# Performance work log

Measured on AMD Instinct MI355X. Metric: run time of the kernel, lower is better.

The kernel has to match this reference:

```python
import jax, jax.numpy as jnp
import numpy as np

# LIF hyperparameters (match init_kwargs)
DT = 1.0
TAU = 20.0
THRESHOLD = 1.0
RESET = 0.0
REST = 0.0
REFR_PERIOD = 2.0
LOW_BOUND = -1.0
KOEFF = float(np.exp(-DT / TAU))  # membrane decay per step
N = 2048
N_IN = 512
N_OUT = 256
B = 64
T = 512


def setup_inputs() -> dict:
    key = jax.random.key(0)
    k1, k2 = jax.random.split(key)
    # Binary input spike trains [B, n_in, T] (uint8 semantics, stored as float32)
    inp = (jax.random.uniform(k1, (B, N_IN, T)) < 0.2).astype(jnp.float32)
    # Dense synaptic weight matrix W [N, N]; row i = incoming weights of neuron i
    W = jax.random.normal(k2, (N, N), dtype=jnp.float32) * (0.1 / np.sqrt(N))
    return {"inp": inp, "W": W}


def reference(inp, W):
    batch, n_in, time = inp.shape
    n = W.shape[0]
    xs = jnp.moveaxis(inp, 2, 0)  # [T, B, n_in]

    def step(carry, x_t):
        state, refr, out_t = carry  # state/refr/out_t: [B, N]
        # Inject input spikes into the first n_in output slots
        out_t = out_t.at[:, :n_in].set(x_t)
        # LIF update: decay toward rest + synaptic input W @ out_t
        state = (state - REST) * KOEFF + REST + jnp.einsum('ij,bj->bi', W, out_t)
        # Refractory neurons clamped to reset potential
        state = jnp.where(refr > 0, RESET, state)
        spike = state >= THRESHOLD
        refr = refr - DT
        refr = jnp.where(spike, REFR_PERIOD, refr)
        # Lower-bound clamp on membrane potential
        state = jnp.where(state < LOW_BOUND, LOW_BOUND, state)
        out_t = spike.astype(jnp.float32)
        return (state, refr, out_t), out_t[:, -N_OUT:]

    init = (jnp.zeros((batch, n), jnp.float32),
            jnp.zeros((batch, n), jnp.float32),
            jnp.zeros((batch, n), jnp.float32))
    _, outs = jax.lax.scan(step, init, xs)  # outs: [T, B, n_out]
    return jnp.transpose(outs, (1, 2, 0))  # [B, n_out, T]
```

## Files before the change

### kernel.cpp

```cpp
#include <hip/hip_runtime.h>

#define KOEFF 0.951229424500714f
#define KP2   0.904837418035960f
#define KP4   0.818730753077982f
#define KP8   0.670320046035639f
#define KP16  0.449328964117222f
#define K64   0.040762203978366f
#define LOG2K (-0.07213475204444817f)

typedef unsigned short u16;
typedef __attribute__((ext_vector_type(8))) short short8;
typedef __attribute__((ext_vector_type(4))) float f32x4;

__device__ __forceinline__ u16 f2bf(float f) {
  unsigned int v = __float_as_uint(f);
  unsigned int r = (v + 0x7FFFu + ((v >> 16) & 1u)) >> 16;
  return (u16)r;
}

__global__ __launch_bounds__(256) void k_prep(const float* __restrict__ X, const float* __restrict__ W,
                                              u16* __restrict__ XT, u16* __restrict__ Whi,
                                              int* __restrict__ flags) {
  __shared__ float tile[64][65];
  const int blk = blockIdx.x;
  if (blk < 4096) {
    const int b  = blk >> 6;
    const int r2 = blk & 63;
    const int j0 = (r2 & 7) * 64;
    const int t0 = (r2 >> 3) * 64;
    const float* src = X + ((size_t)b * 512 + j0) * 512 + t0;
    for (int e = threadIdx.x; e < 64 * 16; e += 256) {
      int r = e >> 4, c = e & 15;
      float4 v = *(const float4*)(src + (size_t)r * 512 + c * 4);
      tile[r][c * 4 + 0] = v.x; tile[r][c * 4 + 1] = v.y;
      tile[r][c * 4 + 2] = v.z; tile[r][c * 4 + 3] = v.w;
    }
    __syncthreads();
    u16* dst = XT + ((size_t)b * 512 + t0) * 512 + j0;
    for (int e = threadIdx.x; e < 64 * 16; e += 256) {
      int tr = e >> 4, c = e & 15;
      ushort4 o;
      o.x = f2bf(tile[c * 4 + 0][tr]); o.y = f2bf(tile[c * 4 + 1][tr]);
      o.z = f2bf(tile[c * 4 + 2][tr]); o.w = f2bf(tile[c * 4 + 3][tr]);
      *(ushort4*)(dst + (size_t)tr * 512 + c * 4) = o;
    }
  } else {
    if (blk == 4096 && threadIdx.x < 64) flags[threadIdx.x] = 0;
    int p = (blk - 4096) * 256 + threadIdx.x;
    int i = p >> 9, j = p & 511;
    Whi[p] = f2bf(W[(size_t)(512 + i) * 2048 + j]);
  }
}

__global__ __launch_bounds__(1024) void k_fused(const u16* __restrict__ A, const u16* __restrict__ Bx,
                                                float* __restrict__ out, int* __restrict__ flags) {
  __shared__ u16 lA[128 * 64];
  __shared__ u16 lB[512 * 64];
  __shared__ float Pl[8 * 128];
  const int mt   = blockIdx.x;
  const int b    = blockIdx.y;
  const int tid  = threadIdx.x;
  const int wv   = tid >> 6;
  const int lane = tid & 63;
  const int tl   = lane & 15;
  const int qg   = lane >> 4;
  const int l7   = lane & 7;
  const int c    = wv & 7;
  const int h    = wv >> 3;

  f32x4 acc[4][4];
#pragma unroll
  for (int mi = 0; mi < 4; ++mi)
#pragma unroll
    for (int ni = 0; ni < 4; ++ni) acc[mi][ni] = (f32x4)0.0f;

  const u16* gA = A + (size_t)mt * 128 * 512;
  const u16* gB = Bx + (size_t)b * 512 * 512;

  const int r    = tid >> 3;
  const int kc   = tid & 7;
  const int soff = r * 512 + ((kc ^ (r & 7)) << 3);

  for (int k0 = 0; k0 < 512; k0 += 64) {
    __syncthreads();
    __builtin_amdgcn_global_load_lds(
        (const __attribute__((address_space(1))) void*)(gA + soff + k0),
        (__attribute__((address_space(3))) void*)(lA + wv * 512), 16, 0, 0);
#pragma unroll
    for (int it = 0; it < 4; ++it) {
      __builtin_amdgcn_global_load_lds(
          (const __attribute__((address_space(1))) void*)(gB + it * 65536 + soff + k0),
          (__attribute__((address_space(3))) void*)(lB + it * 8192 + wv * 512), 16, 0, 0);
    }
    __syncthreads();
#pragma unroll
    for (int ks = 0; ks < 2; ++ks) {
      short8 ah[4], bb[4];
      const int kx = (((ks << 2) | qg) ^ l7) << 3;
#pragma unroll
      for (int mi = 0; mi < 4; ++mi)
        ah[mi] = *(const short8*)&lA[(h * 64 + mi * 16 + tl) * 64 + kx];
#pragma unroll
      for (int ni = 0; ni < 4; ++ni)
        bb[ni] = *(const short8*)&lB[(c * 64 + ni * 16 + tl) * 64 + kx];
#pragma unroll
      for (int mi = 0; mi < 4; ++mi)
#pragma unroll
        for (int ni = 0; ni < 4; ++ni)
          acc[mi][ni] = __builtin_amdgcn_mfma_f32_16x16x32_bf16(ah[mi], bb[ni], acc[mi][ni], 0, 0, 0);
    }
  }
  __syncthreads();

  {
    const float kd[4] = {KOEFF, KP2, KP4, KP8};
    const int   dd[4] = {1, 2, 4, 8};
#pragma unroll
    for (int rd = 0; rd < 4; ++rd) {
      const float kw = kd[rd];
      const int   dl = dd[rd];
#pragma unroll
      for (int mi = 0; mi < 4; ++mi)
#pragma unroll
        for (int ni = 0; ni < 4; ++ni) {
#pragma unroll
          for (int q = 0; q < 4; ++q) {
            float g = __shfl_up(acc[mi][ni][q], dl, 16);
            if (tl < dl) g = 0.f;
            acc[mi][ni][q] = fmaf(kw, g, acc[mi][ni][q]);
          }
        }
    }
  }

#pragma unroll
  for (int mi = 0; mi < 4; ++mi)
#pragma unroll
    for (int q = 0; q < 4; ++q) {
      float b0 = __shfl(acc[mi][0][q], 15, 16);
      float b1 = __shfl(acc[mi][1][q], 15, 16);
      float b2 = __shfl(acc[mi][2][q], 15, 16);
      float b3 = __shfl(acc[mi][3][q], 15, 16);
      float T = fmaf(fmaf(fmaf(b0, KP16, b1), KP16, b2), KP16, b3);
      if (tl == 0) Pl[c * 128 + h * 64 + mi * 16 + qg * 4 + q] = T;
    }
  __syncthreads();

  const float kp = KOEFF * exp2f(LOG2K * (float)tl);
  const bool isout = (mt >= 10);
  bool viol = false;
#pragma unroll
  for (int mi = 0; mi < 4; ++mi) {
#pragma unroll
    for (int q = 0; q < 4; ++q) {
      const int nl = h * 64 + mi * 16 + qg * 4 + q;
      float cr = 0.f;
      for (int d = 0; d < c; ++d) cr = fmaf(cr, K64, Pl[d * 128 + nl]);
      const int gn = mt * 128 + nl;
#pragma unroll
      for (int ni = 0; ni < 4; ++ni) {
        float S = fmaf(kp, cr, acc[mi][ni][q]);
        bool sp = (S >= 1.0f);
        viol = viol || sp || (S < -1.0f);
        if (isout)
          out[((size_t)b * 256 + (gn - 1280)) * 512 + c * 64 + ni * 16 + tl] = sp ? 1.f : 0.f;
        cr = __shfl(S, 15, 16);
      }
    }
  }
  if (viol) atomicOr(&flags[b], 1);
}

__global__ __launch_bounds__(256) void k_fix(const float* __restrict__ X, const float* __restrict__ W,
                                             const int* __restrict__ flags, float* __restrict__ out) {
  const int b = blockIdx.x;
  if (flags[b] == 0) return;
  const int tid = threadIdx.x;
  const int wv = tid >> 6, lane = tid & 63;
  float st[6], rf[6];
#pragma unroll
  for (int r = 0; r < 6; ++r) { st[r] = 0.f; rf[r] = 0.f; }
  __shared__ unsigned int mask[64];
  for (int w = tid; w < 64; w += 256) mask[w] = 0u;
  __syncthreads();
  for (int t = 0; t < 512; ++t) {
    {
      float x = X[((size_t)b * 512 + tid) * 512 + t];
      unsigned long long bl = __ballot(x > 0.5f);
      if (lane == 0) { mask[2 * wv] = (unsigned int)bl; mask[2 * wv + 1] = (unsigned int)(bl >> 32); }
      x = X[((size_t)b * 512 + 256 + tid) * 512 + t];
      bl = __ballot(x > 0.5f);
      if (lane == 0) { mask[8 + 2 * wv] = (unsigned int)bl; mask[9 + 2 * wv] = (unsigned int)(bl >> 32); }
    }
    __syncthreads();
    float add[6] = {0.f, 0.f, 0.f, 0.f, 0.f, 0.f};
    for (int wd = 0; wd < 64; ++wd) {
      unsigned int m = mask[wd];
      while (m) {
        int bitp = __ffs(m) - 1;
        m &= m - 1;
        int j = wd * 32 + bitp;
#pragma unroll
        for (int r = 0; r < 6; ++r) add[r] += W[(size_t)(512 + tid + 256 * r) * 2048 + j];
      }
    }
    bool sp[6];
#pragma unroll
    for (int r = 0; r < 6; ++r) {
      float a = fmaf(st[r], KOEFF, add[r]);
      if (rf[r] > 0.f) a = 0.f;
      sp[r] = a >= 1.0f;
      rf[r] -= 1.f;
      if (sp[r]) rf[r] = 2.f;
      if (a < -1.f) a = -1.f;
      st[r] = a;
      int gi = 512 + tid + 256 * r;
      if (gi >= 1792) out[((size_t)b * 256 + (gi - 1792)) * 512 + t] = sp[r] ? 1.f : 0.f;
    }
    __syncthreads();
#pragma unroll
    for (int r = 0; r < 6; ++r) {
      unsigned long long bl = __ballot(sp[r]);
      if (lane == 0) {
        mask[16 + 8 * r + 2 * wv] = (unsigned int)bl;
        mask[17 + 8 * r + 2 * wv] = (unsigned int)(bl >> 32);
      }
    }
    __syncthreads();
  }
}

__global__ __launch_bounds__(256) void k_exact(const float* __restrict__ X, const float* __restrict__ W,
                                               float* __restrict__ out) {
  const int b = blockIdx.x, tid = threadIdx.x;
  const int wv = tid >> 6, lane = tid & 63;
  float st[6], rf[6];
#pragma unroll
  for (int r = 0; r < 6; ++r) { st[r] = 0.f; rf[r] = 0.f; }
  __shared__ unsigned int mask[64];
  for (int w = tid; w < 64; w += 256) mask[w] = 0u;
  __syncthreads();
  for (int t = 0; t < 512; ++t) {
    {
      float x = X[((size_t)b * 512 + tid) * 512 + t];
      unsigned long long bl = __ballot(x > 0.5f);
      if (lane == 0) { mask[2 * wv] = (unsigned int)bl; mask[2 * wv + 1] = (unsigned int)(bl >> 32); }
      x = X[((size_t)b * 512 + 256 + tid) * 512 + t];
      bl = __ballot(x > 0.5f);
      if (lane == 0) { mask[8 + 2 * wv] = (unsigned int)bl; mask[9 + 2 * wv] = (unsigned int)(bl >> 32); }
    }
    __syncthreads();
    float add[6] = {0.f, 0.f, 0.f, 0.f, 0.f, 0.f};
    for (int wd = 0; wd < 64; ++wd) {
      unsigned int m = mask[wd];
      while (m) {
        int bitp = __ffs(m) - 1;
        m &= m - 1;
        int j = wd * 32 + bitp;
#pragma unroll
        for (int r = 0; r < 6; ++r) add[r] += W[(size_t)(512 + tid + 256 * r) * 2048 + j];
      }
    }
    bool sp[6];
#pragma unroll
    for (int r = 0; r < 6; ++r) {
      float a = fmaf(st[r], KOEFF, add[r]);
      if (rf[r] > 0.f) a = 0.f;
      sp[r] = a >= 1.0f;
      rf[r] -= 1.f;
      if (sp[r]) rf[r] = 2.f;
      if (a < -1.f) a = -1.f;
      st[r] = a;
      int gi = 512 + tid + 256 * r;
      if (gi >= 1792) out[((size_t)b * 256 + (gi - 1792)) * 512 + t] = sp[r] ? 1.f : 0.f;
    }
    __syncthreads();
#pragma unroll
    for (int r = 0; r < 6; ++r) {
      unsigned long long bl = __ballot(sp[r]);
      if (lane == 0) {
        mask[16 + 8 * r + 2 * wv] = (unsigned int)bl;
        mask[17 + 8 * r + 2 * wv] = (unsigned int)(bl >> 32);
      }
    }
    __syncthreads();
  }
}

extern "C" void kernel_launch(void* const* d_in, const int* in_sizes, int n_in,
                              void* d_out, int out_size, void* d_ws, size_t ws_size,
                              hipStream_t stream) {
  const float* X = (const float*)d_in[0];
  const float* W = (const float*)d_in[1];
  float* out = (float*)d_out;
  char* ws = (char*)d_ws;

  const size_t SZ_XT = 64ull * 512 * 512 * 2;
  const size_t SZ_WH = 1536ull * 512 * 2;
  const size_t SZ_FL = 256;
  const size_t NEED_FULL = SZ_XT + SZ_WH + SZ_FL;

  if (ws_size >= NEED_FULL) {
    u16* XT  = (u16*)ws;
    u16* Whi = (u16*)(ws + SZ_XT);
    int* FL  = (int*)(ws + SZ_XT + SZ_WH);
    k_prep<<<7168, 256, 0, stream>>>(X, W, XT, Whi, FL);
    k_fused<<<dim3(12, 64), 1024, 0, stream>>>(Whi, XT, out, FL);
    k_fix<<<64, 256, 0, stream>>>(X, W, FL, out);
  } else {
    k_exact<<<64, 256, 0, stream>>>(X, W, out);
  }
}
```

Baseline: 258.1 us.

## Split fused GEMM-scan kernel into smaller GEMM tiles plus interval-check kernel

Replaces the 1024-thread fused kernel, which handled all 512 timesteps per block, with 256-thread blocks that each cover a 128x128 tile along the time axis. Each tile emits its carry-out sum and per-neuron min/max threshold-margin bounds. A separate kernel then zero-fills the output, chains the eight time segments per neuron, and sets the fallback flag if any bound might be crossed, using a small tolerance. This gives four times as many blocks and a smaller LDS footprint, which should improve occupancy and load balance. The cost is an extra launch, more reloads of the W tiles, and round trips through global memory for the P and interval buffers.

```diff
diff --git a/kernel.cpp b/kernel.cpp
--- a/kernel.cpp
+++ b/kernel.cpp
@@ -52,21 +52,21 @@
   }
 }
 
-__global__ __launch_bounds__(1024) void k_fused(const u16* __restrict__ A, const u16* __restrict__ Bx,
-                                                float* __restrict__ out, int* __restrict__ flags) {
+__global__ __launch_bounds__(256) void k_gemm(const u16* __restrict__ A, const u16* __restrict__ Bx,
+                                              float* __restrict__ P, float* __restrict__ IVmin,
+                                              float* __restrict__ IVmax) {
   __shared__ u16 lA[128 * 64];
-  __shared__ u16 lB[512 * 64];
-  __shared__ float Pl[8 * 128];
-  const int mt   = blockIdx.x;
+  __shared__ u16 lB[128 * 64];
   const int b    = blockIdx.y;
+  const int mt   = blockIdx.x >> 2;
+  const int nt   = blockIdx.x & 3;
   const int tid  = threadIdx.x;
   const int wv   = tid >> 6;
   const int lane = tid & 63;
   const int tl   = lane & 15;
   const int qg   = lane >> 4;
   const int l7   = lane & 7;
-  const int c    = wv & 7;
-  const int h    = wv >> 3;
+  const int wr   = wv >> 1, wc = wv & 1;
 
   f32x4 acc[4][4];
 #pragma unroll
@@ -75,100 +75,136 @@
     for (int ni = 0; ni < 4; ++ni) acc[mi][ni] = (f32x4)0.0f;
 
   const u16* gA = A + (size_t)mt * 128 * 512;
-  const u16* gB = Bx + (size_t)b * 512 * 512;
-
-  const int r    = tid >> 3;
-  const int kc   = tid & 7;
-  const int soff = r * 512 + ((kc ^ (r & 7)) << 3);
+  const u16* gB = Bx + ((size_t)b * 512 + nt * 128) * 512;
 
   for (int k0 = 0; k0 < 512; k0 += 64) {
-    __syncthreads();
-    __builtin_amdgcn_global_load_lds(
-        (const __attribute__((address_space(1))) void*)(gA + soff + k0),
-        (__attribute__((address_space(3))) void*)(lA + wv * 512), 16, 0, 0);
 #pragma unroll
     for (int it = 0; it < 4; ++it) {
+      int byteoff = wv * 4096 + it * 1024 + lane * 16;
+      int row   = byteoff >> 7;
+      int chunk = (byteoff >> 4) & 7;
+      int ksub  = (chunk ^ (row & 7)) * 8;
+      int ldsoff = wv * 2048 + it * 512;
       __builtin_amdgcn_global_load_lds(
-          (const __attribute__((address_space(1))) void*)(gB + it * 65536 + soff + k0),
-          (__attribute__((address_space(3))) void*)(lB + it * 8192 + wv * 512), 16, 0, 0);
-    }
-    __syncthreads();
-#pragma unroll
-    for (int ks = 0; ks < 2; ++ks) {
+          (const __attribute__((address_space(1))) void*)(gA + (size_t)row * 512 + k0 + ksub),
+          (__attribute__((address_space(3))) void*)(lA + ldsoff), 16, 0, 0);
+      __builtin_amdgcn_global_load_lds(
+          (const __attribute__((address_space(1))) void*)(gB + (size_t)row * 512 + k0 + ksub),
+          (__attribute__((address_space(3))) void*)(lB + ldsoff), 16, 0, 0);
+    }
+    __syncthreads();
+#pragma unroll
+    for (int kk = 0; kk < 2; ++kk) {
       short8 ah[4], bb[4];
-      const int kx = (((ks << 2) | qg) ^ l7) << 3;
-#pragma unroll
-      for (int mi = 0; mi < 4; ++mi)
-        ah[mi] = *(const short8*)&lA[(h * 64 + mi * 16 + tl) * 64 + kx];
-#pragma unroll
-      for (int ni = 0; ni < 4; ++ni)
-        bb[ni] = *(const short8*)&lB[(c * 64 + ni * 16 + tl) * 64 + kx];
+      const int kc = kk * 4 + qg;
+#pragma unroll
+      for (int mi = 0; mi < 4; ++mi) {
+        int m = wr * 64 + mi * 16 + tl;
+        ah[mi] = *(const short8*)&lA[m * 64 + (((kc ^ l7) & 7) << 3)];
+      }
+#pragma unroll
+      for (int ni = 0; ni < 4; ++ni) {
+        int n = wc * 64 + ni * 16 + tl;
+        bb[ni] = *(const short8*)&lB[n * 64 + (((kc ^ l7) & 7) << 3)];
+      }
 #pragma unroll
       for (int mi = 0; mi < 4; ++mi)
 #pragma unroll
         for (int ni = 0; ni < 4; ++ni)
           acc[mi][ni] = __builtin_amdgcn_mfma_f32_16x16x32_bf16(ah[mi], bb[ni], acc[mi][ni], 0, 0, 0);
     }
-  }
-  __syncthreads();
+    __syncthreads();
+  }
 
   {
+    const int c = nt * 2 + wc;
     const float kd[4] = {KOEFF, KP2, KP4, KP8};
     const int   dd[4] = {1, 2, 4, 8};
 #pragma unroll
     for (int rd = 0; rd < 4; ++rd) {
       const float kw = kd[rd];
-      const int   dl = dd[rd];
+      const int dl = dd[rd];
 #pragma unroll
       for (int mi = 0; mi < 4; ++mi)
 #pragma unroll
-        for (int ni = 0; ni < 4; ++ni) {
+        for (int ni = 0; ni < 4; ++ni)
 #pragma unroll
           for (int q = 0; q < 4; ++q) {
             float g = __shfl_up(acc[mi][ni][q], dl, 16);
             if (tl < dl) g = 0.f;
             acc[mi][ni][q] = fmaf(kw, g, acc[mi][ni][q]);
           }
+    }
+    const float kp  = exp2f(LOG2K * (float)(tl + 1));
+    const float krt = exp2f(-LOG2K * (float)(tl + 1));
+    const float K16R[4] = {1.f, 2.225540928f, 4.953032424f, 11.02317638f};
+    float cmn[4][4], cmx[4][4], Pv[4][4];
+#pragma unroll
+    for (int mi = 0; mi < 4; ++mi)
+#pragma unroll
+      for (int q = 0; q < 4; ++q) {
+        float pc = 0.f;
+        float cmin_v = 3.4e38f, cmax_v = -3.4e38f;
+#pragma unroll
+        for (int ni = 0; ni < 4; ++ni) {
+          float sl = fmaf(kp, pc, acc[mi][ni][q]);
+          float kr = krt * K16R[ni];
+          cmin_v = fminf(cmin_v, (1.0f - sl) * kr);
+          cmax_v = fmaxf(cmax_v, (-1.0f - sl) * kr);
+          pc = fmaf(pc, KP16, __shfl(acc[mi][ni][q], 15, 16));
         }
-    }
-  }
-
-#pragma unroll
-  for (int mi = 0; mi < 4; ++mi)
-#pragma unroll
-    for (int q = 0; q < 4; ++q) {
-      float b0 = __shfl(acc[mi][0][q], 15, 16);
-      float b1 = __shfl(acc[mi][1][q], 15, 16);
-      float b2 = __shfl(acc[mi][2][q], 15, 16);
-      float b3 = __shfl(acc[mi][3][q], 15, 16);
-      float T = fmaf(fmaf(fmaf(b0, KP16, b1), KP16, b2), KP16, b3);
-      if (tl == 0) Pl[c * 128 + h * 64 + mi * 16 + qg * 4 + q] = T;
-    }
-  __syncthreads();
-
-  const float kp = KOEFF * exp2f(LOG2K * (float)tl);
-  const bool isout = (mt >= 10);
-  bool viol = false;
-#pragma unroll
-  for (int mi = 0; mi < 4; ++mi) {
-#pragma unroll
-    for (int q = 0; q < 4; ++q) {
-      const int nl = h * 64 + mi * 16 + qg * 4 + q;
-      float cr = 0.f;
-      for (int d = 0; d < c; ++d) cr = fmaf(cr, K64, Pl[d * 128 + nl]);
-      const int gn = mt * 128 + nl;
-#pragma unroll
-      for (int ni = 0; ni < 4; ++ni) {
-        float S = fmaf(kp, cr, acc[mi][ni][q]);
-        bool sp = (S >= 1.0f);
-        viol = viol || sp || (S < -1.0f);
-        if (isout)
-          out[((size_t)b * 256 + (gn - 1280)) * 512 + c * 64 + ni * 16 + tl] = sp ? 1.f : 0.f;
-        cr = __shfl(S, 15, 16);
-      }
-    }
-  }
-  if (viol) atomicOr(&flags[b], 1);
+        Pv[mi][q] = pc;
+        cmn[mi][q] = cmin_v;
+        cmx[mi][q] = cmax_v;
+      }
+#pragma unroll
+    for (int off = 1; off < 16; off <<= 1)
+#pragma unroll
+      for (int mi = 0; mi < 4; ++mi)
+#pragma unroll
+        for (int q = 0; q < 4; ++q) {
+          cmn[mi][q] = fminf(cmn[mi][q], __shfl_xor(cmn[mi][q], off, 16));
+          cmx[mi][q] = fmaxf(cmx[mi][q], __shfl_xor(cmx[mi][q], off, 16));
+        }
+    if (tl == 0) {
+      const size_t base = ((size_t)b * 8 + c) * 1536 + mt * 128 + wr * 64 + (qg << 2);
+#pragma unroll
+      for (int mi = 0; mi < 4; ++mi)
+#pragma unroll
+        for (int q = 0; q < 4; ++q) {
+          P[base + mi * 16 + q]     = Pv[mi][q];
+          IVmin[base + mi * 16 + q] = cmn[mi][q];
+          IVmax[base + mi * 16 + q] = cmx[mi][q];
+        }
+    }
+  }
+}
+
+__global__ __launch_bounds__(256) void k_check(const float* __restrict__ P, const float* __restrict__ IVmin,
+                                               const float* __restrict__ IVmax, float* __restrict__ out,
+                                               int* __restrict__ flags) {
+  const int blk = blockIdx.x;
+  if (blk < 384) {
+    float4 z = make_float4(0.f, 0.f, 0.f, 0.f);
+    float4* o = (float4*)out;
+    for (int idx = blk * 256 + threadIdx.x; idx < 64 * 256 * 512 / 4; idx += 384 * 256)
+      o[idx] = z;
+  } else {
+    const int g = (blk - 384) * 256 + threadIdx.x;
+    const int b = g / 1536;
+    const int i = g - b * 1536;
+    const size_t base = (size_t)b * 8 * 1536 + i;
+    float c = 0.f;
+    bool viol = false;
+#pragma unroll
+    for (int d = 0; d < 8; ++d) {
+      float hi = IVmin[base + (size_t)d * 1536];
+      float lo = IVmax[base + (size_t)d * 1536];
+      viol = viol || (c >= hi - 1e-3f) || (c <= lo + 1e-3f);
+      c = fmaf(c, K64, P[base + (size_t)d * 1536]);
+    }
+    if (viol) atomicOr(&flags[b], 1);
+  }
 }
 
 __global__ __launch_bounds__(256) void k_fix(const float* __restrict__ X, const float* __restrict__ W,
@@ -297,15 +333,20 @@
 
   const size_t SZ_XT = 64ull * 512 * 512 * 2;
   const size_t SZ_WH = 1536ull * 512 * 2;
+  const size_t SZ_P  = 64ull * 8 * 1536 * 4;
   const size_t SZ_FL = 256;
-  const size_t NEED_FULL = SZ_XT + SZ_WH + SZ_FL;
+  const size_t NEED_FULL = SZ_XT + SZ_WH + 3 * SZ_P + SZ_FL;
 
   if (ws_size >= NEED_FULL) {
-    u16* XT  = (u16*)ws;
-    u16* Whi = (u16*)(ws + SZ_XT);
-    int* FL  = (int*)(ws + SZ_XT + SZ_WH);
+    u16*   XT   = (u16*)ws;
+    u16*   Whi  = (u16*)(ws + SZ_XT);
+    float* P    = (float*)(ws + SZ_XT + SZ_WH);
+    float* IVmn = (float*)(ws + SZ_XT + SZ_WH + SZ_P);
+    float* IVmx = (float*)(ws + SZ_XT + SZ_WH + 2 * SZ_P);
+    int*   FL   = (int*)(ws + SZ_XT + SZ_WH + 3 * SZ_P);
     k_prep<<<7168, 256, 0, stream>>>(X, W, XT, Whi, FL);
-    k_fused<<<dim3(12, 64), 1024, 0, stream>>>(Whi, XT, out, FL);
+    k_gemm<<<dim3(48, 64), 256, 0, stream>>>(Whi, XT, P, IVmn, IVmx);
+    k_check<<<768, 256, 0, stream>>>(P, IVmn, IVmx, out, FL);
     k_fix<<<64, 256, 0, stream>>>(X, W, FL, out);
   } else {
     k_exact<<<64, 256, 0, stream>>>(X, W, out);
```

New measurement: 245.4 us. 4.9% less time.
